# Kernel optimization log

Hardware: AMD Instinct MI355X
Metric: run time of the kernel (lower is better)

Reference implementation:

```python
import jax, jax.numpy as jnp
import numpy as np

N = 16384; E = 262144; B = 32; H = 128; R = 50; L = 4; CUTOFF = 5.0

def _lin(x, w, b):
    return x @ w + b

def _mlp2(x, w1, b1, w2, b2):
    return _lin(jax.nn.silu(_lin(x, w1, b1)), w2, b2)

def _ln(x, g, b):
    m = x.mean(-1, keepdims=True)
    v = ((x - m) ** 2).mean(-1, keepdims=True)
    return (x - m) / jnp.sqrt(v + 1e-5) * g + b

def setup_inputs() -> dict:
    key = jax.random.key(0)
    ks = iter(jax.random.split(key, 64))
    def w(shape):
        fan = shape[-2] if len(shape) >= 2 else shape[-1]
        return jax.random.normal(next(ks), shape, jnp.float32) / np.sqrt(fan)
    z = lambda shape: jnp.zeros(shape, jnp.float32)
    return {
        'atomic_numbers': jax.random.randint(next(ks), (N,), 0, 100, dtype=jnp.int32),
        'pos': 2.0 * jax.random.normal(next(ks), (N, 3), jnp.float32),
        'batch': jnp.sort(jax.random.randint(next(ks), (N,), 0, B, dtype=jnp.int32)),
        'edge_index': jax.random.randint(next(ks), (2, E), 0, N, dtype=jnp.int32),
        'embed': w((100, H)),
        'widths': jnp.full((R,), 0.5, jnp.float32),
        'ee_w1': w((L, R, H)), 'ee_b1': z((L, H)), 'ee_w2': w((L, H, H)), 'ee_b2': z((L, H)),
        'msg_w1': w((L, 3 * H, H)), 'msg_b1': z((L, H)), 'msg_w2': w((L, H, H)), 'msg_b2': z((L, H)),
        'gate_w': w((L, H, H)), 'gate_b': z((L, H)),
        'upd_w1': w((L, 2 * H, H)), 'upd_b1': z((L, H)), 'upd_w2': w((L, H, H)), 'upd_b2': z((L, H)),
        'ln_g': jnp.ones((L, H), jnp.float32), 'ln_b': z((L, H)),
        'gp_w1': w((H, H)), 'gp_b1': z((H,)), 'gp_w2': w((H, 1)), 'gp_b2': z((1,)),
        'pn_w': w((H, H)), 'pn_b': z((H,)),
        'ro_w1': w((H, H)), 'ro_b1': z((H,)), 'ro_w2': w((H, H)), 'ro_b2': z((H,)),
    }

def reference(atomic_numbers, pos, batch, edge_index, embed, widths,
              ee_w1, ee_b1, ee_w2, ee_b2, msg_w1, msg_b1, msg_w2, msg_b2,
              gate_w, gate_b, upd_w1, upd_b1, upd_w2, upd_b2, ln_g, ln_b,
              gp_w1, gp_b1, gp_w2, gp_b2, pn_w, pn_b, ro_w1, ro_b1, ro_w2, ro_b2):
    src, dst = edge_index[0], edge_index[1]  # x_j = x[src], x_i = x[dst]
    x = embed[atomic_numbers]                          # [N,H]
    # GaussianBasis RBF with cosine cutoff
    d = jnp.linalg.norm(pos[dst] - pos[src], axis=-1)[:, None]  # [E,1]
    centers = jnp.linspace(0.0, CUTOFF, R)
    gamma = 1.0 / (2.0 * widths ** 2)
    rbf = jnp.exp(-gamma * (d - centers) ** 2)
    cut = 0.5 * (jnp.cos(np.pi * d / CUTOFF) + 1.0) * (d < CUTOFF).astype(x.dtype)
    edge_attr = rbf * cut                              # [E,R]
    feats = [x]
    for l in range(L):
        ee = _mlp2(edge_attr, ee_w1[l], ee_b1[l], ee_w2[l], ee_b2[l])          # [E,H]
        m_in = jnp.concatenate([x[dst], x[src], ee], axis=-1)                   # [E,3H]
        msg = _mlp2(m_in, msg_w1[l], msg_b1[l], msg_w2[l], msg_b2[l])           # [E,H]
        gate = jax.nn.sigmoid(_lin(ee, gate_w[l], gate_b[l]))
        aggr = jax.ops.segment_sum(msg * gate, dst, num_segments=N)             # [N,H]
        upd = _mlp2(jnp.concatenate([aggr, x], axis=-1), upd_w1[l], upd_b1[l], upd_w2[l], upd_b2[l])
        x = _ln(x + upd, ln_g[l], ln_b[l])
        feats.append(x)
    atom_features = (feats[-3] + feats[-2] + feats[-1]) / 3.0                   # mean of last 3
    atom_embeddings = _mlp2(atom_features, ro_w1, ro_b1, ro_w2, ro_b2)
    # AttentionalAggregation: softmax(gate_nn(x)) over nodes per graph, weighted sum of nn(x)
    g = _lin(jnp.tanh(_lin(atom_embeddings, gp_w1, gp_b1)), gp_w2, gp_b2)[:, 0] # [N]
    gmax = jax.ops.segment_max(g, batch, num_segments=B)
    gmax = jnp.where(jnp.isfinite(gmax), gmax, 0.0)
    ex = jnp.exp(g - gmax[batch])
    den = jax.ops.segment_sum(ex, batch, num_segments=B)
    alpha = ex / den[batch]
    h = jax.nn.silu(_lin(atom_embeddings, pn_w, pn_b))
    graph_atom_features = jax.ops.segment_sum(alpha[:, None] * h, batch, num_segments=B)
    return atom_features, atom_embeddings, graph_atom_features
```

## Files before the change

### kernel.cpp

```cpp
#include <hip/hip_runtime.h>

#define NN   16384
#define NE   262144
#define NB   32
#define H    128
#define NH   (NN*H)
#define RBF  50
#define TM   64
#define KC   64
#define KP   72
#define HBP  136
#define CHW  9216
#define LT2  115712
#define LN_  49152
#define NG   196608
#define EPB  128
#define WEV  32
#define TT   4096
#define PB   32

typedef unsigned short u16;
typedef short bf16x8 __attribute__((ext_vector_type(8)));
typedef float f32x4 __attribute__((ext_vector_type(4)));
typedef float f32x16 __attribute__((ext_vector_type(16)));
// ... 40 lines not shown
  x = q.x; y = q.y;
#else
  int l_ = (int)(threadIdx.x & 63);
  unsigned as_ = __shfl(a, l_^32);
  unsigned bs_ = __shfl(b, l_^32);
  x = (l_ < 32) ? a : bs_;
  y = (l_ < 32) ? as_ : b;
#endif
}

__device__ __forceinline__ void pack_frags(const float* v, uint4& f0, uint4& f1){
  unsigned P0 = pk2(v[0],v[1]),   P1 = pk2(v[2],v[3]);
  unsigned P2 = pk2(v[4],v[5]),   P3 = pk2(v[6],v[7]);
  unsigned P4 = pk2(v[8],v[9]),   P5 = pk2(v[10],v[11]);
  unsigned P6 = pk2(v[12],v[13]), P7 = pk2(v[14],v[15]);
  unsigned x0,y0,x1,y1,x2,y2,x3,y3;
  plswap(P0,P2,x0,y0); plswap(P1,P3,x1,y1);
  plswap(P4,P6,x2,y2); plswap(P5,P7,x3,y3);
  f0.x=x0; f0.y=x1; f0.z=y0; f0.w=y1;
  f1.x=x2; f1.y=x3; f1.z=y2; f1.w=y3;
}

__device__ __forceinline__ void gll16(const u16* g, u16* l){
  __builtin_amdgcn_global_load_lds((const __attribute__((address_space(1))) void*)g,
                                   (__attribute__((address_space(3))) void*)l, 16, 0, 0);
}
__device__ __forceinline__ void gll4(const u16* g, u16* l){
  __builtin_amdgcn_global_load_lds((const __attribute__((address_space(1))) void*)g,
                                   (__attribute__((address_space(3))) void*)l, 4, 0, 0);
}

__global__ void k_zero(float* __restrict__ p, int n){
  int i = blockIdx.x*256 + threadIdx.x; if (i < n) p[i] = 0.f;
}
__global__ void k_zero_i(int* __restrict__ p, int n){
  int i = blockIdx.x*256 + threadIdx.x; if (i < n) p[i] = 0;
}
__global__ void k_embed(const int* __restrict__ z, const float* __restrict__ emb,
                        float* __restrict__ x, u16* __restrict__ xb){
  int i = blockIdx.x*256 + threadIdx.x;
  int n = i >> 7, h = i & 127;
  float v = emb[z[n]*H + h];
  x[i] = v; xb[i] = f2bf(v);
}

__global__ void k_pack(const float* __restrict__ ee_w1, const float* __restrict__ ee_w2,
                       const float* __restrict__ msg_w1, const float* __restrict__ msg_w2,
                       const float* __restrict__ gate_w, u16* __restrict__ out){
  int idx = blockIdx.x*256 + threadIdx.x;
  int l = blockIdx.y;
  if (idx >= LT2) return;
  u16* o = out + (size_t)l*LT2;
  float v = 0.f;
  if (idx < 82944){
    int c = idx / CHW, r = idx % CHW, row = r / 72, col = r % 72;
    if (col < 64){
      if (c == 0)      v = (col < RBF) ? ee_w1[(size_t)l*RBF*H + col*H + row] : 0.f;
      else if (c <= 2) v = ee_w2 [(size_t)l*H*H + (64*(c-1)+col)*H + row];
      else if (c <= 4) v = msg_w1[(size_t)l*3*H*H + (256 + 64*(c-3)+col)*H + row];
      else if (c <= 6) v = gate_w[(size_t)l*H*H + (64*(c-5)+col)*H + row];
      else             v = msg_w2[(size_t)l*H*H + (64*(c-7)+col)*H + row];
    }
  } else if (idx < 99328){
    int j = idx - 82944; int row = j >> 7, k = j & 127;
    v = msg_w1[(size_t)l*3*H*H + k*H + row];
  } else {
    int j = idx - 99328; int row = j >> 7, k = j & 127;
    v = msg_w1[(size_t)l*3*H*H + (128+k)*H + row];
  }
  o[idx] = f2bf(v);
}

__global__ void k_packn(const float* __restrict__ upd_w1, const float* __restrict__ upd_w2,
                        const float* __restrict__ ro_w1, const float* __restrict__ ro_w2,
                        const float* __restrict__ pn_w, const float* __restrict__ gp_w1,
                        u16* __restrict__ out){
  int idx = blockIdx.x*256 + threadIdx.x;
  if (idx >= NG + 65536) return;
  float v;
  if (idx < NG){
    int l = idx / LN_, j = idx % LN_;
    if (j < 32768){ int c = j>>8, k = j&255; v = upd_w1[(size_t)l*256*H + k*H + c]; }
    else { int j2 = j-32768; int c = j2>>7, k = j2&127; v = upd_w2[(size_t)l*H*H + k*H + c]; }
  } else {
    int j = idx - NG; int m = j >> 14; int j2 = j & 16383;
    int c = j2>>7, k = j2&127;
    const float* W = (m==0) ? ro_w1 : (m==1) ? ro_w2 : (m==2) ? pn_w : gp_w1;
    v = W[k*H + c];
  }
  out[idx] = f2bf(v);
}

__global__ void k_hist(const int* __restrict__ dstv, int* __restrict__ cnt){
  int e = blockIdx.x*256 + threadIdx.x;
  if (e < NE) atomicAdd(&cnt[dstv[e]], 1);
}
__global__ __launch_bounds__(1024)
void k_scan(int* __restrict__ cnt, int* __restrict__ start){
  __shared__ int ps[1024];
  int tid = threadIdx.x;
  int base = tid*16;
  int loc[16]; int s = 0;
#pragma unroll
  for (int i=0;i<16;i++){ loc[i] = s; s += cnt[base+i]; }
  ps[tid] = s; __syncthreads();
  for (int off=1; off<1024; off<<=1){
    int v = (tid>=off) ? ps[tid-off] : 0;
    __syncthreads();
    ps[tid] += v;
    __syncthreads();
  }
  int pre = (tid>0) ? ps[tid-1] : 0;
#pragma unroll
  for (int i=0;i<16;i++){ int v = pre + loc[i]; start[base+i] = v; cnt[base+i] = v; }
  if (tid == 0) start[NN] = NE;
}
__global__ void k_scatter(const int* __restrict__ srcv, const int* __restrict__ dstv,
                          int* __restrict__ cursor, int* __restrict__ src_s,
                          int* __restrict__ dst_s){
  int e = blockIdx.x*256 + threadIdx.x;
  if (e >= NE) return;
  int d = dstv[e];
  int p = atomicAdd(&cursor[d], 1);
  src_s[p] = srcv[e]; dst_s[p] = d;
}

#define TMFMA(CHP, AOFF, ACC) \
  _Pragma("unroll") \
  for (int ks_=0; ks_<64; ks_+=32){ \
    bf16x8 bf_ = *(const bf16x8*)&Ab[wrow + l15][(AOFF) + ks_ + q8]; \
    _Pragma("unroll") \
    for (int t_=0;t_<8;t_++){ \
      bf16x8 wf_ = *(const bf16x8*)&(CHP)[(t_*16 + l15)*72 + ks_ + q8]; \
      ACC[t_] = __builtin_amdgcn_mfma_f32_16x16x32_bf16(wf_, bf_, ACC[t_], 0, 0, 0); \
    } \
  }

__global__ __launch_bounds__(256)
void k_table(const u16* __restrict__ packw, const float* __restrict__ widths,
             const float* __restrict__ ee_b1, const float* __restrict__ ee_b2,
             const float* __restrict__ gate_b,
// ... 37 lines not shown
    uint4 u1; u1.x=vv[4]; u1.y=vv[5]; u1.z=vv[6]; u1.w=vv[7];
    *(uint4*)&Ab[r][k0]   = u0;
    *(uint4*)&Ab[r][k0+8] = u1;
  }
  __syncthreads();
  f32x4 acc[8];
#pragma unroll
  for (int t=0;t<8;t++) acc[t] = (f32x4)(0.f);
  TMFMA(CH[0], 0, acc)
  const int s = rowbase + wrow + l15;
#pragma unroll
  for (int t=0;t<8;t++){
    int co = t*16 + quad*4;
    int po = (co>>6)*KP + (co&63);
    *(uint2*)&Ab[wrow + l15][po] = pack4(
      siluf_(acc[t][0]+b1s[co]),   siluf_(acc[t][1]+b1s[co+1]),
      siluf_(acc[t][2]+b1s[co+2]), siluf_(acc[t][3]+b1s[co+3]));
  }
#pragma unroll
  for (int t=0;t<8;t++) acc[t] = (f32x4)(0.f);
  TMFMA(CH[1], 0, acc)
  TMFMA(CH[2], KP, acc)
#pragma unroll
  for (int t=0;t<8;t++){
    int co = t*16 + quad*4;
    int po = (co>>6)*KP + (co&63);
    *(uint2*)&Ab[wrow + l15][po] = pack4(
      acc[t][0]+b2s[co], acc[t][1]+b2s[co+1], acc[t][2]+b2s[co+2], acc[t][3]+b2s[co+3]);
  }
#pragma unroll
  for (int t=0;t<8;t++) acc[t] = (f32x4)(0.f);
  TMFMA(CH[3], 0, acc)
  TMFMA(CH[4], KP, acc)
#pragma unroll
  for (int t=0;t<8;t++){
    int co = t*16 + quad*4;
    *(uint2*)&m1t[((size_t)lyr*TT + s)*H + permc(co)] =
      pack4(acc[t][0], acc[t][1], acc[t][2], acc[t][3]);
  }
#pragma unroll
  for (int t=0;t<8;t++) acc[t] = (f32x4)(0.f);
  TMFMA(CH[5], 0, acc)
  TMFMA(CH[6], KP, acc)
#pragma unroll
  for (int t=0;t<8;t++){
    int co = t*16 + quad*4;
    *(uint2*)&gt[((size_t)lyr*TT + s)*H + permc(co)] = pack4(
      sigmoidf_(acc[t][0]+bgs[co]),   sigmoidf_(acc[t][1]+bgs[co+1]),
      sigmoidf_(acc[t][2]+bgs[co+2]), sigmoidf_(acc[t][3]+bgs[co+3]));
  }
}


#define GSTAGE(cidx, dbuf) { \
  const u16* gs_ = pw + (size_t)(cidx)*CHW; \
  u16* ls_ = &UN[(dbuf)*CHW]; \
  _Pragma("unroll") \
  for (int i_=0;i_<4;i_++) \
    gll16(gs_ + (i_*256 + tid)*8, ls_ + (i_*256 + tid)*8); \
  _Pragma("unroll") \
  for (int i_=0;i_<2;i_++) \
    gll4(gs_ + 8192 + (i_*256 + tid)*2, ls_ + 8192 + (i_*256 + tid)*2); \
}

#define ECHUNK32(WB, FR, ACC) \
  _Pragma("unroll") \
  for (int s_=0; s_<4; s_++){ \
    bf16x8 bf_ = __builtin_bit_cast(bf16x8, (FR)[s_]); \
    _Pragma("unroll") \
    for (int t_=0;t_<4;t_++){ \
      bf16x8 wf_ = *(const bf16x8*)&(WB)[(t_*32 + l31)*72 + s_*16 + hi8]; \
      ACC[t_] = __builtin_amdgcn_mfma_f32_32x32x16_bf16(wf_, bf_, ACC[t_], 0, 0, 0); \
    } \
  }

#define ZACC(A) { _Pragma("unroll") for (int z_=0;z_<4;z_++) A[z_] = (f32x16)(0.f); }

#define SEL2(V, UF) (((UF)&1) ? make_uint2((V).z,(V).w) : make_uint2((V).x,(V).y))

#define DWEL(r) (((r)&3)==0 ? dw[(r)>>2].x : ((r)&3)==1 ? dw[(r)>>2].y : \
                 ((r)&3)==2 ? dw[(r)>>2].z : dw[(r)>>2].w)

__global__ __launch_bounds__(256, 3)
void k_edge(const int* __restrict__ src_s, const int* __restrict__ dst_s,
            const float* __restrict__ pos,
            const u16* __restrict__ y1b, const u16* __restrict__ y2b,
            const u16* __restrict__ pw,
            const u16* __restrict__ m1t, const u16* __restrict__ gt,
            const float* __restrict__ b_m2, float* __restrict__ aggr){
  __shared__ __align__(16) u16 UN[2*CHW];
  __shared__ float BM[H];
  const int tid = threadIdx.x;
  const int wave = tid>>6, l = tid&63, l31 = l&31, hi = l>>5, hi8 = hi*8;
  const int ebase = blockIdx.x*EPB + wave*WEV;
  const int eid   = ebase + l31;
  if (tid < H) BM[tid] = b_m2[tid];

  const int esrc = src_s[eid], edst = dst_s[eid];
  float dx = pos[3*edst]   - pos[3*esrc];
  float dy = pos[3*edst+1] - pos[3*esrc+1];
  float dz = pos[3*edst+2] - pos[3*esrc+2];
  float dist = sqrtf(dx*dx + dy*dy + dz*dz);
  float uu = fminf(dist, 5.0f) * ((float)(TT-1)/5.0f);
  int i0 = (int)uu; if (i0 > TT-2) i0 = TT-2;
  float w = uu - (float)i0;

  const u16* yp1 = y1b + (size_t)edst*H + hi*64;
  const u16* yp2 = y2b + (size_t)esrc*H + hi*64;
  const u16* mp  = m1t + (size_t)i0*H  + hi*64;
  uint4 Y1[8], Y2[8], M0[8], M1[8];
#pragma unroll
  for (int i=0;i<8;i++){
    Y1[i] = *(const uint4*)&yp1[i*8];
    Y2[i] = *(const uint4*)&yp2[i*8];
    M0[i] = *(const uint4*)&mp[i*8];
    M1[i] = *(const uint4*)&mp[H + i*8];
  }

  GSTAGE(0,0)
  GSTAGE(1,1)

  uint4 fmh[8];
#pragma unroll
  for (int tf=0;tf<4;tf++){
    float v_[16];
#pragma unroll
    for (int uf=0;uf<4;uf++){
      int iv = 2*tf + (uf>>1);
      uint2 a1 = SEL2(Y1[iv],uf), a2 = SEL2(Y2[iv],uf);
      uint2 m0 = SEL2(M0[iv],uf), m1 = SEL2(M1[iv],uf);
      float p0 = blo(m0.x), p1 = bhi(m0.x), p2 = blo(m0.y), p3 = bhi(m0.y);
      float q0 = blo(m1.x), q1 = bhi(m1.x), q2 = blo(m1.y), q3 = bhi(m1.y);
      v_[4*uf+0] = siluf_(fmaf(w, q0-p0, p0) + blo(a1.x) + blo(a2.x));
      v_[4*uf+1] = siluf_(fmaf(w, q1-p1, p1) + bhi(a1.x) + bhi(a2.x));
      v_[4*uf+2] = siluf_(fmaf(w, q2-p2, p2) + blo(a1.y) + blo(a2.y));
      v_[4*uf+3] = siluf_(fmaf(w, q3-p3, p3) + bhi(a1.y) + bhi(a2.y));
    }
    pack_frags(v_, fmh[2*tf], fmh[2*tf+1]);
  }

  __syncthreads();

  const u16* gp = gt + (size_t)i0*H + hi*64;
  uint4 G0[8], G1[8];
#pragma unroll
  for (int i=0;i<8;i++){
    G0[i] = *(const uint4*)&gp[i*8];
    G1[i] = *(const uint4*)&gp[H + i*8];
  }

  f32x16 acc[4];
  ZACC(acc)
  ECHUNK32((&UN[0]),   fmh,   acc)
  ECHUNK32((&UN[CHW]), fmh+4, acc)

  __syncthreads();
  u16* Sb = &UN[wave*(WEV*HBP)];

#pragma unroll
  for (int tf=0;tf<4;tf++){
#pragma unroll
    for (int uf=0;uf<4;uf++){
      int iv = 2*tf + (uf>>1);
      int co = 32*tf + 4*hi + 8*uf;
      float4 bm = *(const float4*)&BM[co];
      uint2 a0 = SEL2(G0[iv],uf), a1 = SEL2(G1[iv],uf);
      float g0 = fmaf(w, blo(a1.x)-blo(a0.x), blo(a0.x));
      float g1 = fmaf(w, bhi(a1.x)-bhi(a0.x), bhi(a0.x));
      float g2 = fmaf(w, blo(a1.y)-blo(a0.y), blo(a0.y));
      float g3 = fmaf(w, bhi(a1.y)-bhi(a0.y), bhi(a0.y));
      float m0 = (acc[tf][4*uf+0]+bm.x)*g0;
      float m1 = (acc[tf][4*uf+1]+bm.y)*g1;
      float m2 = (acc[tf][4*uf+2]+bm.z)*g2;
      float m3 = (acc[tf][4*uf+3]+bm.w)*g3;
      *(uint2*)&Sb[l31*HBP + co] = pack4(m0, m1, m2, m3);
    }
  }

  {
    int4 dw[8];
#pragma unroll
    for (int i=0;i<8;i++) dw[i] = *(const int4*)&dst_s[ebase + 4*i];
    int c0 = l*2;
    float a0 = 0.f, a1 = 0.f;
    int cur = dw[0].x;
#pragma unroll
    for (int r=0;r<32;r++){
      int d = DWEL(r);
      if (d != cur){
        atomicAdd(&aggr[(size_t)cur*H + c0],     a0);
        atomicAdd(&aggr[(size_t)cur*H + c0 + 1], a1);
        a0 = 0.f; a1 = 0.f; cur = d;
      }
      unsigned pv = *(const unsigned*)&Sb[r*HBP + c0];
      a0 += blo(pv); a1 += bhi(pv);
    }
    atomicAdd(&aggr[(size_t)cur*H + c0],     a0);
    atomicAdd(&aggr[(size_t)cur*H + c0 + 1], a1);
  }
}


#define NMFMA(AB, WB, NP, ACC) \
  _Pragma("unroll") \
  for (int kk_=0; kk_<(NP)*64; kk_+=32){ \
    int po_ = (kk_>>6)*KP + (kk_&63); \
    bf16x8 bf_ = *(const bf16x8*)&AB[wrow + l15][po_ + q8]; \
    _Pragma("unroll") \
    for (int t_=0;t_<8;t_++){ \
      bf16x8 wf_ = *(const bf16x8*)&WB[t_*16 + l15][po_ + q8]; \
      ACC[t_] = __builtin_amdgcn_mfma_f32_16x16x32_bf16(wf_, bf_, ACC[t_], 0, 0, 0); \
    } \
  }

#define NMFMA2(AB, AOFF, WB_, WOFF, ACC) \
  _Pragma("unroll") \
  for (int kk_=0; kk_<64; kk_+=32){ \
    bf16x8 bf_ = *(const bf16x8*)&AB[wrow + l15][(AOFF) + kk_ + q8]; \
    _Pragma("unroll") \
    for (int t_=0;t_<8;t_++){ \
      bf16x8 wf_ = *(const bf16x8*)&WB_[t_*16 + l15][(WOFF) + kk_ + q8]; \
      ACC[t_] = __builtin_amdgcn_mfma_f32_16x16x32_bf16(wf_, bf_, ACC[t_], 0, 0, 0); \
    } \
  }

#define NSTAGE_W2(WB_, GSRC, KPAD, SP, DP) \
  _Pragma("unroll") \
  for (int i_=0;i_<4;i_++){ \
    int o_ = tid + i_*256; int c_ = o_>>3, ko_ = (o_&7)*8; \
    *(uint4*)&WB_[c_][(DP)*KP + ko_] = *(const uint4*)((GSRC) + (size_t)c_*(KPAD) + (SP)*64 + ko_); \
  }
#define NSTAGE_W(WB, GSRC, KPAD, P) NSTAGE_W2(WB, GSRC, KPAD, P, P)

#define NSTAGE_A(AB, GSRC, P) \
  _Pragma("unroll") \
  for (int i_=0;i_<2;i_++){ \
    int o_ = tid*2 + i_; int r_ = o_>>3, ko_ = (o_&7)*8; \
    *(uint4*)&AB[r_][(P)*KP + ko_] = *(const uint4*)((GSRC) + (size_t)r_*H + (P)*64 + ko_); \
  }

#define NSTAGE_AF(AB, GSRC, P) \
  _Pragma("unroll") \
  for (int i_=0;i_<2;i_++){ \
    int o_ = tid*2 + i_; int r_ = o_>>3, ko_ = (o_&7)*8; \
    const float* rp_ = (GSRC) + (size_t)r_*H + (P)*64 + ko_; \
    float4 f0_ = *(const float4*)rp_; \
    float4 f1_ = *(const float4*)(rp_ + 4); \
    uint4 pk_; \
    pk_.x = pk2(f0_.x, f0_.y); pk_.y = pk2(f0_.z, f0_.w); \
    pk_.z = pk2(f1_.x, f1_.y); pk_.w = pk2(f1_.z, f1_.w); \
    *(uint4*)&AB[r_][(P)*KP + ko_] = pk_; \
  }

__global__ __launch_bounds__(256)
void k_y12(const u16* __restrict__ xb, const u16* __restrict__ Wd,
           const u16* __restrict__ Ws, const float* __restrict__ b1,
           u16* __restrict__ y1, u16* __restrict__ y2){
  __shared__ u16 Ab[TM][2*KP];
  __shared__ u16 W1[H][2*KP];
  __shared__ u16 W2[H][2*KP];
  __shared__ float bls[H];
  const int tid = threadIdx.x;
  const int wave = tid>>6, l = tid&63, l15 = l&15, quad = l>>4;
  const int wrow = wave*16, q8 = quad*8;
  const int rowbase = blockIdx.x*TM;
  if (tid < H) bls[tid] = b1[tid];
  NSTAGE_W(W1, Wd, 128, 0) NSTAGE_W(W1, Wd, 128, 1)
  NSTAGE_W(W2, Ws, 128, 0) NSTAGE_W(W2, Ws, 128, 1)
  NSTAGE_A(Ab, xb + (size_t)rowbase*H, 0) NSTAGE_A(Ab, xb + (size_t)rowbase*H, 1)
  __syncthreads();
  f32x4 a1[8], a2[8];
#pragma unroll
  for (int t=0;t<8;t++){ a1[t] = (f32x4)(0.f); a2[t] = (f32x4)(0.f); }
  NMFMA(Ab, W1, 2, a1)
  NMFMA(Ab, W2, 2, a2)
  const int node = rowbase + wrow + l15;
#pragma unroll
  for (int t=0;t<8;t++){
    int co = t*16 + quad*4;
    int pc = permc(co);
    *(uint2*)&y1[(size_t)node*H + pc] = pack4(
      a1[t][0]+bls[co], a1[t][1]+bls[co+1], a1[t][2]+bls[co+2], a1[t][3]+bls[co+3]);
    *(uint2*)&y2[(size_t)node*H + pc] = pack4(
      a2[t][0], a2[t][1], a2[t][2], a2[t][3]);
  }
}

template<int ADDSUM, int DOY12>
__global__ __launch_bounds__(256)
void k_upd(float* __restrict__ aggr, const u16* __restrict__ xin,
           const u16* __restrict__ W1p, const float* __restrict__ b1,
           const u16* __restrict__ W2p, const float* __restrict__ b2,
           const float* __restrict__ lng, const float* __restrict__ lnb,
           float* __restrict__ x, float* __restrict__ sumf, u16* __restrict__ xb,
           const u16* __restrict__ Wdn, const u16* __restrict__ Wsn,
           const float* __restrict__ b1n,
           u16* __restrict__ y1, u16* __restrict__ y2){
  __shared__ u16 Ab[TM][4*KP];
  __shared__ u16 WB[3][H][2*KP];
  __shared__ float bls[H], b2s[H], lgs[H], lbs[H], b1s[H];
  const int tid = threadIdx.x;
  const int wave = tid>>6, l = tid&63, l15 = l&15, quad = l>>4;
  const int wrow = wave*16, q8 = quad*8;
  const int rowbase = blockIdx.x*TM;
  if (tid < H){ bls[tid] = b1[tid]; b2s[tid] = b2[tid]; lgs[tid] = lng[tid];
                if (DOY12) b1s[tid] = b1n[tid]; }
  else lbs[tid-H] = lnb[tid-H];
  NSTAGE_W2(WB[0], W1p, 256, 0, 0) NSTAGE_W2(WB[0], W1p, 256, 1, 1)
  NSTAGE_W2(WB[1], W1p, 256, 2, 0) NSTAGE_W2(WB[1], W1p, 256, 3, 1)
  NSTAGE_W2(WB[2], W2p, 128, 0, 0) NSTAGE_W2(WB[2], W2p, 128, 1, 1)
  NSTAGE_AF(Ab, aggr + (size_t)rowbase*H, 0)
  NSTAGE_AF(Ab, aggr + (size_t)rowbase*H, 1)
  {
    const u16* xs = xin + (size_t)rowbase*H - 128;
    NSTAGE_A(Ab, xs, 2) NSTAGE_A(Ab, xs, 3)
  }
  __syncthreads();
  f32x4 acc[8];
#pragma unroll
  for (int t=0;t<8;t++) acc[t] = (f32x4)(0.f);
  NMFMA2(Ab, 0,    WB[0], 0,  acc)
  NMFMA2(Ab, KP,   WB[0], KP, acc)
  NMFMA2(Ab, 2*KP, WB[1], 0,  acc)
  NMFMA2(Ab, 3*KP, WB[1], KP, acc)
  {
    float4 z = make_float4(0.f,0.f,0.f,0.f);
#pragma unroll
    for (int i=0;i<8;i++){
      int o = tid + i*256;
      *(float4*)&aggr[(size_t)rowbase*H + (size_t)o*4] = z;
    }
  }
#pragma unroll
  for (int t=0;t<8;t++){
    int co = t*16 + quad*4;
    int po = (co>>6)*KP + (co&63);
    *(uint2*)&Ab[wrow + l15][po] = pack4(
      siluf_(acc[t][0]+bls[co]),   siluf_(acc[t][1]+bls[co+1]),
      siluf_(acc[t][2]+bls[co+2]), siluf_(acc[t][3]+bls[co+3]));
  }
  __syncthreads();
  if (DOY12){
    NSTAGE_W2(WB[0], Wdn, 128, 0, 0) NSTAGE_W2(WB[0], Wdn, 128, 1, 1)
    NSTAGE_W2(WB[1], Wsn, 128, 0, 0) NSTAGE_W2(WB[1], Wsn, 128, 1, 1)
  }
#pragma unroll
  for (int t=0;t<8;t++) acc[t] = (f32x4)(0.f);
  NMFMA2(Ab, 0,  WB[2], 0,  acc)
  NMFMA2(Ab, KP, WB[2], KP, acc)
  const int node = rowbase + wrow + l15;
  const size_t ro = (size_t)node*H;
  float y[8][4]; float s = 0.f, ss = 0.f;
#pragma unroll
  for (int t=0;t<8;t++){
    int co = t*16 + quad*4;
    float4 xv = *(const float4*)&x[ro + co];
    y[t][0] = xv.x + acc[t][0] + b2s[co];
    y[t][1] = xv.y + acc[t][1] + b2s[co+1];
    y[t][2] = xv.z + acc[t][2] + b2s[co+2];
    y[t][3] = xv.w + acc[t][3] + b2s[co+3];
#pragma unroll
    for (int r=0;r<4;r++){ s += y[t][r]; ss += y[t][r]*y[t][r]; }
  }
  s  += __shfl_xor(s, 16);  s  += __shfl_xor(s, 32);
  ss += __shfl_xor(ss, 16); ss += __shfl_xor(ss, 32);
  float mean = s*(1.0f/H);
  float var  = ss*(1.0f/H) - mean*mean;
  float inv  = rsqrtf(var + 1e-5f);
#pragma unroll
  for (int t=0;t<8;t++){
    int co = t*16 + quad*4;
    float4 o;
    o.x = (y[t][0]-mean)*inv*lgs[co]   + lbs[co];
    o.y = (y[t][1]-mean)*inv*lgs[co+1] + lbs[co+1];
    o.z = (y[t][2]-mean)*inv*lgs[co+2] + lbs[co+2];
    o.w = (y[t][3]-mean)*inv*lgs[co+3] + lbs[co+3];
    *(float4*)&x[ro + co] = o;
    if (ADDSUM){
      float4 sf = *(const float4*)&sumf[ro + co];
      sf.x += o.x*(1.0f/3.0f); sf.y += o.y*(1.0f/3.0f);
      sf.z += o.z*(1.0f/3.0f); sf.w += o.w*(1.0f/3.0f);
      *(float4*)&sumf[ro + co] = sf;
      if (!DOY12)
        *(uint2*)&y1[ro + co] = pack4(sf.x, sf.y, sf.z, sf.w);
    }
    *(uint2*)&xb[ro + co] = pack4(o.x, o.y, o.z, o.w);
    y[t][0] = o.x; y[t][1] = o.y; y[t][2] = o.z; y[t][3] = o.w;
  }

  if (DOY12){
#pragma unroll
    for (int t=0;t<8;t++){
      int co = t*16 + quad*4;
      int po = (2 + (co>>6))*KP + (co&63);
      *(uint2*)&Ab[wrow + l15][po] = pack4(y[t][0], y[t][1], y[t][2], y[t][3]);
    }
    __syncthreads();
    f32x4 a1[8], a2[8];
#pragma unroll
    for (int t=0;t<8;t++){ a1[t] = (f32x4)(0.f); a2[t] = (f32x4)(0.f); }
    NMFMA2(Ab, 2*KP, WB[0], 0,  a1)
    NMFMA2(Ab, 3*KP, WB[0], KP, a1)
    NMFMA2(Ab, 2*KP, WB[1], 0,  a2)
    NMFMA2(Ab, 3*KP, WB[1], KP, a2)
#pragma unroll
    for (int t=0;t<8;t++){
      int co = t*16 + quad*4;
      int pc = permc(co);
      *(uint2*)&y1[ro + pc] = pack4(
        a1[t][0]+b1s[co], a1[t][1]+b1s[co+1], a1[t][2]+b1s[co+2], a1[t][3]+b1s[co+3]);
      *(uint2*)&y2[ro + pc] = pack4(a2[t][0], a2[t][1], a2[t][2], a2[t][3]);
    }
  }
}

__global__ __launch_bounds__(256)
void k_tail(const u16* __restrict__ afb,
            const u16* __restrict__ Wro1, const float* __restrict__ bro1,
            const u16* __restrict__ Wro2, const float* __restrict__ bro2,
            const u16* __restrict__ Wpn,  const float* __restrict__ bpn,
            const u16* __restrict__ Wgp,  const float* __restrict__ bgp,
            const float* __restrict__ w2, const float* __restrict__ b2g,
            float* __restrict__ out_ae, u16* __restrict__ hb,
            float* __restrict__ g){
  __shared__ u16 Ab[TM][2*KP];
  __shared__ u16 WB[3][H][2*KP];
  __shared__ float r1b[H], r2b[H], pnb[H], g1b[H], w2s[H];
  const int tid = threadIdx.x;
  const int wave = tid>>6, l = tid&63, l15 = l&15, quad = l>>4;
  const int wrow = wave*16, q8 = quad*8;
  const int rowbase = blockIdx.x*TM;
  if (tid < H){ r1b[tid]=bro1[tid]; r2b[tid]=bro2[tid]; pnb[tid]=bpn[tid]; g1b[tid]=bgp[tid]; }
  else w2s[tid-H] = w2[tid-H];
  NSTAGE_W(WB[0], Wro1, 128, 0) NSTAGE_W(WB[0], Wro1, 128, 1)
  NSTAGE_W(WB[1], Wro2, 128, 0) NSTAGE_W(WB[1], Wro2, 128, 1)
  NSTAGE_W(WB[2], Wpn,  128, 0) NSTAGE_W(WB[2], Wpn,  128, 1)
  NSTAGE_A(Ab, afb + (size_t)rowbase*H, 0) NSTAGE_A(Ab, afb + (size_t)rowbase*H, 1)
  __syncthreads();
  f32x4 acc[8];
#pragma unroll
  for (int t=0;t<8;t++) acc[t] = (f32x4)(0.f);
  NMFMA2(Ab, 0, WB[0], 0, acc) NMFMA2(Ab, KP, WB[0], KP, acc)
#pragma unroll
  for (int t=0;t<8;t++){
    int co = t*16 + quad*4;
    int po = (co>>6)*KP + (co&63);
    *(uint2*)&Ab[wrow + l15][po] = pack4(
      siluf_(acc[t][0]+r1b[co]),   siluf_(acc[t][1]+r1b[co+1]),
      siluf_(acc[t][2]+r1b[co+2]), siluf_(acc[t][3]+r1b[co+3]));
  }
  __syncthreads();
  NSTAGE_W(WB[0], Wgp, 128, 0) NSTAGE_W(WB[0], Wgp, 128, 1)
#pragma unroll
  for (int t=0;t<8;t++) acc[t] = (f32x4)(0.f);
  NMFMA2(Ab, 0, WB[1], 0, acc) NMFMA2(Ab, KP, WB[1], KP, acc)
  const int node = rowbase + wrow + l15;
  const size_t ro = (size_t)node*H;
#pragma unroll
  for (int t=0;t<8;t++){
    int co = t*16 + quad*4;
    float v0 = acc[t][0]+r2b[co],   v1 = acc[t][1]+r2b[co+1];
    float v2 = acc[t][2]+r2b[co+2], v3 = acc[t][3]+r2b[co+3];
    float4 o; o.x=v0; o.y=v1; o.z=v2; o.w=v3;
    *(float4*)&out_ae[ro + co] = o;
    int po = (co>>6)*KP + (co&63);
    *(uint2*)&Ab[wrow + l15][po] = pack4(v0,v1,v2,v3);
  }
  asm volatile("s_waitcnt lgkmcnt(0)" ::: "memory");
#pragma unroll
  for (int t=0;t<8;t++) acc[t] = (f32x4)(0.f);
  NMFMA2(Ab, 0, WB[2], 0, acc) NMFMA2(Ab, KP, WB[2], KP, acc)
#pragma unroll
  for (int t=0;t<8;t++){
    int co = t*16 + quad*4;
    *(uint2*)&hb[ro + co] = pack4(
      siluf_(acc[t][0]+pnb[co]),   siluf_(acc[t][1]+pnb[co+1]),
      siluf_(acc[t][2]+pnb[co+2]), siluf_(acc[t][3]+pnb[co+3]));
  }
  __syncthreads();
#pragma unroll
  for (int t=0;t<8;t++) acc[t] = (f32x4)(0.f);
  NMFMA2(Ab, 0, WB[0], 0, acc) NMFMA2(Ab, KP, WB[0], KP, acc)
  float p = 0.f;
#pragma unroll
  for (int t=0;t<8;t++){
    int co = t*16 + quad*4;
#pragma unroll
    for (int r=0;r<4;r++) p = fmaf(tanhf(acc[t][r]+g1b[co+r]), w2s[co+r], p);
  }
  p += __shfl_xor(p, 16); p += __shfl_xor(p, 32);
  if (quad == 0) g[node] = p + b2g[0];
}

__global__ void k_start(const int* __restrict__ batch, int* __restrict__ start){
  int b = threadIdx.x;
  if (b > NB) return;
  if (b == NB){ start[NB] = NN; return; }
  int lo = 0, hi = NN;
  while (lo < hi){ int mid = (lo+hi) >> 1; if (batch[mid] < b) lo = mid+1; else hi = mid; }
  start[b] = lo;
}

__global__ __launch_bounds__(256)
void k_pool(const int* __restrict__ start, const float* __restrict__ g,
            const u16* __restrict__ hb, float* __restrict__ out){
  const int b   = blockIdx.x / PB;
  const int sub = blockIdx.x % PB;
  const int s = start[b], e = start[b+1];
  const int tid = threadIdx.x;
  __shared__ float red[4];
  __shared__ float s_gmax, s_den;
  __shared__ float part[2][H];

  float mx = -1e30f;
  for (int n = s + tid; n < e; n += 256) mx = fmaxf(mx, g[n]);
#pragma unroll
  for (int m=32;m>=1;m>>=1) mx = fmaxf(mx, __shfl_xor(mx, m, 64));
  if ((tid & 63) == 0) red[tid >> 6] = mx;
  __syncthreads();
  if (tid == 0){
    float v = fmaxf(fmaxf(red[0],red[1]), fmaxf(red[2],red[3]));
    s_gmax = (e > s) ? v : 0.0f;
  }
  __syncthreads();
  const float gmax = s_gmax;

  float sum = 0.f;
  for (int n = s + tid; n < e; n += 256) sum += __expf(g[n] - gmax);
#pragma unroll
  for (int m=32;m>=1;m>>=1) sum += __shfl_xor(sum, m, 64);
  if ((tid & 63) == 0) red[tid >> 6] = sum;
  __syncthreads();
  if (tid == 0) s_den = red[0]+red[1]+red[2]+red[3];
  __syncthreads();
  const float den = s_den;
// ... 48 lines not shown
  const float* gp_b2  = (const float*)d_in[25];
  const float* pn_w   = (const float*)d_in[26];
  const float* pn_b   = (const float*)d_in[27];
  const float* ro_w1  = (const float*)d_in[28];
  const float* ro_b1  = (const float*)d_in[29];
  const float* ro_w2  = (const float*)d_in[30];
  const float* ro_b2  = (const float*)d_in[31];

  const int* srcv = ei;
  const int* dstv = ei + NE;

  char* p0 = (char*)d_ws;
  char* p = p0;
  auto carve = [&](size_t bytes)->char*{ char* q = p; p += (bytes + 63) & ~(size_t)63; return q; };
  float* x     = (float*)carve((size_t)NH*4);
  float* aggr  = (float*)carve((size_t)NH*4);
  float* gsc   = (float*)carve((size_t)NN*4);
  float* exb   = (float*)carve((size_t)NN*4);
  int*   startb  = (int*)carve((size_t)(NB+2)*4);
  int*   estart  = (int*)carve((size_t)(NN+1)*4);
  int*   ecursor = (int*)carve((size_t)NN*4);
  int*   src_s   = (int*)carve((size_t)NE*4);
  int*   dst_s   = (int*)carve((size_t)NE*4);
  u16*   xb      = (u16*)carve((size_t)NH*2);
  u16*   packw   = (u16*)carve((size_t)4*LT2*2);
  u16*   packn   = (u16*)carve((size_t)(NG+65536)*2);
  u16*   nb1     = (u16*)carve((size_t)NH*2);
  u16*   nb2     = (u16*)carve((size_t)NH*2);
  u16*   m1tab   = (u16*)carve((size_t)4*TT*H*2);
  u16*   gtab    = (u16*)carve((size_t)4*TT*H*2);

  float* out_af  = (float*)d_out;
  float* out_ae  = out_af + NH;
  float* out_gaf = out_ae + NH;

  k_pack<<<dim3((LT2+255)/256, 4), 256, 0, stream>>>(ee_w1, ee_w2, msg_w1, msg_w2, gate_w, packw);
  k_packn<<<(NG+65536+255)/256, 256, 0, stream>>>(upd_w1, upd_w2, ro_w1, ro_w2, pn_w, gp_w1, packn);
  k_table<<<dim3(TT/TM, 4), 256, 0, stream>>>(packw, widths, ee_b1, ee_b2, gate_b, m1tab, gtab);
  k_zero_i<<<(NN+255)/256, 256, 0, stream>>>(ecursor, NN);
  k_hist<<<NE/256, 256, 0, stream>>>(dstv, ecursor);
  k_scan<<<1, 1024, 0, stream>>>(ecursor, estart);
  k_scatter<<<NE/256, 256, 0, stream>>>(srcv, dstv, ecursor, src_s, dst_s);
  k_embed<<<NH/256, 256, 0, stream>>>(Z, embed, x, xb);
  k_zero<<<NH/256, 256, 0, stream>>>(out_af, NH);
  k_zero<<<(NB*H+255)/256, 256, 0, stream>>>(out_gaf, NB*H);
  k_zero<<<NH/256, 256, 0, stream>>>(aggr, NH);

  k_y12<<<NN/TM, 256, 0, stream>>>(xb, packw + 82944, packw + 99328, msg_b1, nb1, nb2);

  for (int l=0; l<4; l++){
    const u16* pwn = packn + (size_t)l*LN_;
    const u16* pwN = packw + (size_t)(l+1)*LT2;
    k_edge<<<NE/EPB, 256, 0, stream>>>(src_s, dst_s, pos, nb1, nb2,
                                       packw + (size_t)l*LT2 + (size_t)7*CHW,
                                       m1tab + (size_t)l*TT*H, gtab + (size_t)l*TT*H,
                                       msg_b2 + l*H, aggr);
    if (l == 0)
      k_upd<0,1><<<NN/TM, 256, 0, stream>>>(aggr, xb, pwn, upd_b1 + l*H,
                                            pwn + 32768, upd_b2 + l*H,
                                            ln_g + l*H, ln_b + l*H, x, out_af, xb,
                                            pwN + 82944, pwN + 99328, msg_b1 + (l+1)*H,
                                            nb1, nb2);
    else if (l < 3)
      k_upd<1,1><<<NN/TM, 256, 0, stream>>>(aggr, xb, pwn, upd_b1 + l*H,
                                            pwn + 32768, upd_b2 + l*H,
                                            ln_g + l*H, ln_b + l*H, x, out_af, xb,
                                            pwN + 82944, pwN + 99328, msg_b1 + (l+1)*H,
                                            nb1, nb2);
    else
      k_upd<1,0><<<NN/TM, 256, 0, stream>>>(aggr, xb, pwn, upd_b1 + l*H,
                                            pwn + 32768, upd_b2 + l*H,
                                            ln_g + l*H, ln_b + l*H, x, out_af, xb,
                                            packw, packw, msg_b1,
                                            nb1, nb2);
  }

  k_tail<<<NN/TM, 256, 0, stream>>>(nb1,
                                    packn + NG,         ro_b1,
                                    packn + NG + 16384, ro_b2,
                                    packn + NG + 32768, pn_b,
                                    packn + NG + 49152, gp_b1, gp_w2, gp_b2,
                                    out_ae, nb2, gsc);
  k_start<<<1, 64, 0, stream>>>(batch, startb);
  k_pool<<<NB*PB, 256, 0, stream>>>(startb, gsc, nb2, out_gaf);
}
```

Baseline: 536.7 us.

## Pre-pack weights in MFMA fragment order and read them directly from global

The pack kernels now emit weight matrices already arranged in per-lane MFMA fragment order. The edge, y12, update and tail kernels read weight fragments straight from global memory (L1/L2 cached) instead of staging them into shared memory. This removes the LDS staging copies and several block barriers, and shrinks shared memory so more blocks can be resident (launch bounds raised to 2 blocks per CU). The cost is repeated per-wave global or cache reads of the same weights in every block, which adds L2 traffic, especially in the edge kernel.

```diff
diff --git a/kernel.cpp b/kernel.cpp
--- a/kernel.cpp
+++ b/kernel.cpp
@@ -116,21 +116,34 @@
   if (idx >= LT2) return;
   u16* o = out + (size_t)l*LT2;
   float v = 0.f;
-  if (idx < 82944){
+  if (idx < 64512){
     int c = idx / CHW, r = idx % CHW, row = r / 72, col = r % 72;
     if (col < 64){
       if (c == 0)      v = (col < RBF) ? ee_w1[(size_t)l*RBF*H + col*H + row] : 0.f;
       else if (c <= 2) v = ee_w2 [(size_t)l*H*H + (64*(c-1)+col)*H + row];
       else if (c <= 4) v = msg_w1[(size_t)l*3*H*H + (256 + 64*(c-3)+col)*H + row];
-      else if (c <= 6) v = gate_w[(size_t)l*H*H + (64*(c-5)+col)*H + row];
-      else             v = msg_w2[(size_t)l*H*H + (64*(c-7)+col)*H + row];
-    }
+      else             v = gate_w[(size_t)l*H*H + (64*(c-5)+col)*H + row];
+    }
+  } else if (idx < 64512 + 16384){
+    int r = idx - 64512; int c = r >> 13; int rr = r & 8191;
+    int jj = rr&7, ll = (rr>>3)&63, tt = (rr>>9)&3, ss = (rr>>11)&3;
+    int col = tt*32 + (ll&31);
+    int k = c*64 + ss*16 + (ll>>5)*8 + jj;
+    v = msg_w2[(size_t)l*H*H + k*H + col];
+  } else if (idx < 82944){
+    v = 0.f;
   } else if (idx < 99328){
-    int j = idx - 82944; int row = j >> 7, k = j & 127;
-    v = msg_w1[(size_t)l*3*H*H + k*H + row];
+    int j2 = idx - 82944;
+    int jj=j2&7, ll=(j2>>3)&63, tt=(j2>>9)&7, ks=(j2>>12)&1, pp=j2>>13;
+    int k = pp*64 + ks*32 + (ll>>4)*8 + jj;
+    int col = tt*16 + (ll&15);
+    v = msg_w1[(size_t)l*3*H*H + k*H + col];
   } else {
-    int j = idx - 99328; int row = j >> 7, k = j & 127;
-    v = msg_w1[(size_t)l*3*H*H + (128+k)*H + row];
+    int j2 = idx - 99328;
+    int jj=j2&7, ll=(j2>>3)&63, tt=(j2>>9)&7, ks=(j2>>12)&1, pp=j2>>13;
+    int k = pp*64 + ks*32 + (ll>>4)*8 + jj;
+    int col = tt*16 + (ll&15);
+    v = msg_w1[(size_t)l*3*H*H + (128+k)*H + col];
   }
   o[idx] = f2bf(v);
 }
@@ -144,13 +157,25 @@
   float v;
   if (idx < NG){
     int l = idx / LN_, j = idx % LN_;
-    if (j < 32768){ int c = j>>8, k = j&255; v = upd_w1[(size_t)l*256*H + k*H + c]; }
-    else { int j2 = j-32768; int c = j2>>7, k = j2&127; v = upd_w2[(size_t)l*H*H + k*H + c]; }
+    if (j < 32768){
+      int jj=j&7, ll=(j>>3)&63, tt=(j>>9)&7, ks=(j>>12)&1, pp=j>>13;
+      int k = pp*64 + ks*32 + (ll>>4)*8 + jj;
+      int col = tt*16 + (ll&15);
+      v = upd_w1[(size_t)l*256*H + k*H + col];
+    } else {
+      int j2 = j - 32768;
+      int jj=j2&7, ll=(j2>>3)&63, tt=(j2>>9)&7, ks=(j2>>12)&1, pp=j2>>13;
+      int k = pp*64 + ks*32 + (ll>>4)*8 + jj;
+      int col = tt*16 + (ll&15);
+      v = upd_w2[(size_t)l*H*H + k*H + col];
+    }
   } else {
     int j = idx - NG; int m = j >> 14; int j2 = j & 16383;
-    int c = j2>>7, k = j2&127;
+    int jj=j2&7, ll=(j2>>3)&63, tt=(j2>>9)&7, ks=(j2>>12)&1, pp=j2>>13;
+    int k = pp*64 + ks*32 + (ll>>4)*8 + jj;
+    int col = tt*16 + (ll&15);
     const float* W = (m==0) ? ro_w1 : (m==1) ? ro_w2 : (m==2) ? pn_w : gp_w1;
-    v = W[k*H + c];
+    v = W[k*H + col];
   }
   out[idx] = f2bf(v);
 }
@@ -294,32 +319,8 @@
 }
 
 
-#define GSTAGE(cidx, dbuf) { \
-  const u16* gs_ = pw + (size_t)(cidx)*CHW; \
-  u16* ls_ = &UN[(dbuf)*CHW]; \
-  _Pragma("unroll") \
-  for (int i_=0;i_<4;i_++) \
-    gll16(gs_ + (i_*256 + tid)*8, ls_ + (i_*256 + tid)*8); \
-  _Pragma("unroll") \
-  for (int i_=0;i_<2;i_++) \
-    gll4(gs_ + 8192 + (i_*256 + tid)*2, ls_ + 8192 + (i_*256 + tid)*2); \
-}
-
-#define ECHUNK32(WB, FR, ACC) \
-  _Pragma("unroll") \
-  for (int s_=0; s_<4; s_++){ \
-    bf16x8 bf_ = __builtin_bit_cast(bf16x8, (FR)[s_]); \
-    _Pragma("unroll") \
-    for (int t_=0;t_<4;t_++){ \
-      bf16x8 wf_ = *(const bf16x8*)&(WB)[(t_*32 + l31)*72 + s_*16 + hi8]; \
-      ACC[t_] = __builtin_amdgcn_mfma_f32_32x32x16_bf16(wf_, bf_, ACC[t_], 0, 0, 0); \
-    } \
-  }
-
 #define ZACC(A) { _Pragma("unroll") for (int z_=0;z_<4;z_++) A[z_] = (f32x16)(0.f); }
-
 #define SEL2(V, UF) (((UF)&1) ? make_uint2((V).z,(V).w) : make_uint2((V).x,(V).y))
-
 #define DWEL(r) (((r)&3)==0 ? dw[(r)>>2].x : ((r)&3)==1 ? dw[(r)>>2].y : \
                  ((r)&3)==2 ? dw[(r)>>2].z : dw[(r)>>2].w)
 
@@ -330,12 +331,13 @@
             const u16* __restrict__ pw,
             const u16* __restrict__ m1t, const u16* __restrict__ gt,
             const float* __restrict__ b_m2, float* __restrict__ aggr){
-  __shared__ __align__(16) u16 UN[2*CHW];
+  __shared__ u16 SB[4][WEV][HBP];
   __shared__ float BM[H];
   const int tid = threadIdx.x;
-  const int wave = tid>>6, l = tid&63, l31 = l&31, hi = l>>5, hi8 = hi*8;
+  const int wave = tid>>6, l = tid&63, l31 = l&31, hi = l>>5;
   const int ebase = blockIdx.x*EPB + wave*WEV;
   const int eid   = ebase + l31;
+  u16 (*Sb)[HBP] = SB[wave];
   if (tid < H) BM[tid] = b_m2[tid];
 
   const int esrc = src_s[eid], edst = dst_s[eid];
@@ -359,8 +361,7 @@
     M1[i] = *(const uint4*)&mp[H + i*8];
   }
 
-  GSTAGE(0,0)
-  GSTAGE(1,1)
+  __syncthreads();
 
   uint4 fmh[8];
 #pragma unroll
@@ -381,8 +382,6 @@
     pack_frags(v_, fmh[2*tf], fmh[2*tf+1]);
   }
 
-  __syncthreads();
-
   const u16* gp = gt + (size_t)i0*H + hi*64;
   uint4 G0[8], G1[8];
 #pragma unroll
@@ -393,11 +392,18 @@
 
   f32x16 acc[4];
   ZACC(acc)
-  ECHUNK32((&UN[0]),   fmh,   acc)
-  ECHUNK32((&UN[CHW]), fmh+4, acc)
-
-  __syncthreads();
-  u16* Sb = &UN[wave*(WEV*HBP)];
+#pragma unroll
+  for (int c=0;c<2;c++){
+#pragma unroll
+    for (int s_=0;s_<4;s_++){
+      bf16x8 bf_ = __builtin_bit_cast(bf16x8, fmh[c*4+s_]);
+#pragma unroll
+      for (int t_=0;t_<4;t_++){
+        bf16x8 wf_ = *(const bf16x8*)&pw[((c*16 + s_*4 + t_)*64 + l)*8];
+        acc[t_] = __builtin_amdgcn_mfma_f32_32x32x16_bf16(wf_, bf_, acc[t_], 0, 0, 0);
+      }
+    }
+  }
 
 #pragma unroll
   for (int tf=0;tf<4;tf++){
@@ -415,7 +421,7 @@
       float m1 = (acc[tf][4*uf+1]+bm.y)*g1;
       float m2 = (acc[tf][4*uf+2]+bm.z)*g2;
       float m3 = (acc[tf][4*uf+3]+bm.w)*g3;
-      *(uint2*)&Sb[l31*HBP + co] = pack4(m0, m1, m2, m3);
+      *(uint2*)&Sb[l31][co] = pack4(m0, m1, m2, m3);
     }
   }
 
@@ -434,7 +440,7 @@
         atomicAdd(&aggr[(size_t)cur*H + c0 + 1], a1);
         a0 = 0.f; a1 = 0.f; cur = d;
       }
-      unsigned pv = *(const unsigned*)&Sb[r*HBP + c0];
+      unsigned pv = *(const unsigned*)&Sb[r][c0];
       a0 += blo(pv); a1 += bhi(pv);
     }
     atomicAdd(&aggr[(size_t)cur*H + c0],     a0);
@@ -443,36 +449,19 @@
 }
 
 
-#define NMFMA(AB, WB, NP, ACC) \
+#define GFMFMA(GW, APB, NP, ACC) \
   _Pragma("unroll") \
-  for (int kk_=0; kk_<(NP)*64; kk_+=32){ \
-    int po_ = (kk_>>6)*KP + (kk_&63); \
-    bf16x8 bf_ = *(const bf16x8*)&AB[wrow + l15][po_ + q8]; \
+  for (int p_=0;p_<(NP);p_++){ \
     _Pragma("unroll") \
-    for (int t_=0;t_<8;t_++){ \
-      bf16x8 wf_ = *(const bf16x8*)&WB[t_*16 + l15][po_ + q8]; \
-      ACC[t_] = __builtin_amdgcn_mfma_f32_16x16x32_bf16(wf_, bf_, ACC[t_], 0, 0, 0); \
+    for (int ks_=0;ks_<2;ks_++){ \
+      bf16x8 bf_ = *(const bf16x8*)&Ab[wrow + l15][((APB)+p_)*KP + ks_*32 + q8]; \
+      _Pragma("unroll") \
+      for (int t_=0;t_<8;t_++){ \
+        bf16x8 wf_ = *(const bf16x8*)&(GW)[((((p_*2+ks_)*8)+t_)*64 + l)*8]; \
+        ACC[t_] = __builtin_amdgcn_mfma_f32_16x16x32_bf16(wf_, bf_, ACC[t_], 0, 0, 0); \
+      } \
     } \
   }
-
-#define NMFMA2(AB, AOFF, WB_, WOFF, ACC) \
-  _Pragma("unroll") \
-  for (int kk_=0; kk_<64; kk_+=32){ \
-    bf16x8 bf_ = *(const bf16x8*)&AB[wrow + l15][(AOFF) + kk_ + q8]; \
-    _Pragma("unroll") \
-    for (int t_=0;t_<8;t_++){ \
-      bf16x8 wf_ = *(const bf16x8*)&WB_[t_*16 + l15][(WOFF) + kk_ + q8]; \
-      ACC[t_] = __builtin_amdgcn_mfma_f32_16x16x32_bf16(wf_, bf_, ACC[t_], 0, 0, 0); \
-    } \
-  }
-
-#define NSTAGE_W2(WB_, GSRC, KPAD, SP, DP) \
-  _Pragma("unroll") \
-  for (int i_=0;i_<4;i_++){ \
-    int o_ = tid + i_*256; int c_ = o_>>3, ko_ = (o_&7)*8; \
-    *(uint4*)&WB_[c_][(DP)*KP + ko_] = *(const uint4*)((GSRC) + (size_t)c_*(KPAD) + (SP)*64 + ko_); \
-  }
-#define NSTAGE_W(WB, GSRC, KPAD, P) NSTAGE_W2(WB, GSRC, KPAD, P, P)
 
 #define NSTAGE_A(AB, GSRC, P) \
   _Pragma("unroll") \
@@ -494,28 +483,24 @@
     *(uint4*)&AB[r_][(P)*KP + ko_] = pk_; \
   }
 
-__global__ __launch_bounds__(256)
+__global__ __launch_bounds__(256, 2)
 void k_y12(const u16* __restrict__ xb, const u16* __restrict__ Wd,
            const u16* __restrict__ Ws, const float* __restrict__ b1,
            u16* __restrict__ y1, u16* __restrict__ y2){
   __shared__ u16 Ab[TM][2*KP];
-  __shared__ u16 W1[H][2*KP];
-  __shared__ u16 W2[H][2*KP];
   __shared__ float bls[H];
   const int tid = threadIdx.x;
   const int wave = tid>>6, l = tid&63, l15 = l&15, quad = l>>4;
   const int wrow = wave*16, q8 = quad*8;
   const int rowbase = blockIdx.x*TM;
   if (tid < H) bls[tid] = b1[tid];
-  NSTAGE_W(W1, Wd, 128, 0) NSTAGE_W(W1, Wd, 128, 1)
-  NSTAGE_W(W2, Ws, 128, 0) NSTAGE_W(W2, Ws, 128, 1)
   NSTAGE_A(Ab, xb + (size_t)rowbase*H, 0) NSTAGE_A(Ab, xb + (size_t)rowbase*H, 1)
   __syncthreads();
   f32x4 a1[8], a2[8];
 #pragma unroll
   for (int t=0;t<8;t++){ a1[t] = (f32x4)(0.f); a2[t] = (f32x4)(0.f); }
-  NMFMA(Ab, W1, 2, a1)
-  NMFMA(Ab, W2, 2, a2)
+  GFMFMA(Wd, 0, 2, a1)
+  GFMFMA(Ws, 0, 2, a2)
   const int node = rowbase + wrow + l15;
 #pragma unroll
   for (int t=0;t<8;t++){
@@ -529,17 +514,16 @@
 }
 
 template<int ADDSUM, int DOY12>
-__global__ __launch_bounds__(256)
+__global__ __launch_bounds__(256, 2)
 void k_upd(float* __restrict__ aggr, const u16* __restrict__ xin,
-           const u16* __restrict__ W1p, const float* __restrict__ b1,
-           const u16* __restrict__ W2p, const float* __restrict__ b2,
+           const u16* __restrict__ W1g, const float* __restrict__ b1,
+           const u16* __restrict__ W2g, const float* __restrict__ b2,
            const float* __restrict__ lng, const float* __restrict__ lnb,
            float* __restrict__ x, float* __restrict__ sumf, u16* __restrict__ xb,
            const u16* __restrict__ Wdn, const u16* __restrict__ Wsn,
            const float* __restrict__ b1n,
            u16* __restrict__ y1, u16* __restrict__ y2){
   __shared__ u16 Ab[TM][4*KP];
-  __shared__ u16 WB[3][H][2*KP];
   __shared__ float bls[H], b2s[H], lgs[H], lbs[H], b1s[H];
   const int tid = threadIdx.x;
   const int wave = tid>>6, l = tid&63, l15 = l&15, quad = l>>4;
@@ -548,9 +532,6 @@
   if (tid < H){ bls[tid] = b1[tid]; b2s[tid] = b2[tid]; lgs[tid] = lng[tid];
                 if (DOY12) b1s[tid] = b1n[tid]; }
   else lbs[tid-H] = lnb[tid-H];
-  NSTAGE_W2(WB[0], W1p, 256, 0, 0) NSTAGE_W2(WB[0], W1p, 256, 1, 1)
-  NSTAGE_W2(WB[1], W1p, 256, 2, 0) NSTAGE_W2(WB[1], W1p, 256, 3, 1)
-  NSTAGE_W2(WB[2], W2p, 128, 0, 0) NSTAGE_W2(WB[2], W2p, 128, 1, 1)
   NSTAGE_AF(Ab, aggr + (size_t)rowbase*H, 0)
   NSTAGE_AF(Ab, aggr + (size_t)rowbase*H, 1)
   {
@@ -561,10 +542,7 @@
   f32x4 acc[8];
 #pragma unroll
   for (int t=0;t<8;t++) acc[t] = (f32x4)(0.f);
-  NMFMA2(Ab, 0,    WB[0], 0,  acc)
-  NMFMA2(Ab, KP,   WB[0], KP, acc)
-  NMFMA2(Ab, 2*KP, WB[1], 0,  acc)
-  NMFMA2(Ab, 3*KP, WB[1], KP, acc)
+  GFMFMA(W1g, 0, 4, acc)
   {
     float4 z = make_float4(0.f,0.f,0.f,0.f);
 #pragma unroll
@@ -581,15 +559,9 @@
       siluf_(acc[t][0]+bls[co]),   siluf_(acc[t][1]+bls[co+1]),
       siluf_(acc[t][2]+bls[co+2]), siluf_(acc[t][3]+bls[co+3]));
   }
-  __syncthreads();
-  if (DOY12){
-    NSTAGE_W2(WB[0], Wdn, 128, 0, 0) NSTAGE_W2(WB[0], Wdn, 128, 1, 1)
-    NSTAGE_W2(WB[1], Wsn, 128, 0, 0) NSTAGE_W2(WB[1], Wsn, 128, 1, 1)
-  }
-#pragma unroll
-  for (int t=0;t<8;t++) acc[t] = (f32x4)(0.f);
-  NMFMA2(Ab, 0,  WB[2], 0,  acc)
-  NMFMA2(Ab, KP, WB[2], KP, acc)
+#pragma unroll
+  for (int t=0;t<8;t++) acc[t] = (f32x4)(0.f);
+  GFMFMA(W2g, 0, 2, acc)
   const int node = rowbase + wrow + l15;
   const size_t ro = (size_t)node*H;
   float y[8][4]; float s = 0.f, ss = 0.f;
@@ -637,14 +609,11 @@
       int po = (2 + (co>>6))*KP + (co&63);
       *(uint2*)&Ab[wrow + l15][po] = pack4(y[t][0], y[t][1], y[t][2], y[t][3]);
     }
-    __syncthreads();
     f32x4 a1[8], a2[8];
 #pragma unroll
     for (int t=0;t<8;t++){ a1[t] = (f32x4)(0.f); a2[t] = (f32x4)(0.f); }
-    NMFMA2(Ab, 2*KP, WB[0], 0,  a1)
-    NMFMA2(Ab, 3*KP, WB[0], KP, a1)
-    NMFMA2(Ab, 2*KP, WB[1], 0,  a2)
-    NMFMA2(Ab, 3*KP, WB[1], KP, a2)
+    GFMFMA(Wdn, 2, 2, a1)
+    GFMFMA(Wsn, 2, 2, a2)
 #pragma unroll
     for (int t=0;t<8;t++){
       int co = t*16 + quad*4;
@@ -656,7 +625,7 @@
   }
 }
 
-__global__ __launch_bounds__(256)
+__global__ __launch_bounds__(256, 2)
 void k_tail(const u16* __restrict__ afb,
             const u16* __restrict__ Wro1, const float* __restrict__ bro1,
             const u16* __restrict__ Wro2, const float* __restrict__ bro2,
@@ -666,7 +635,6 @@
             float* __restrict__ out_ae, u16* __restrict__ hb,
             float* __restrict__ g){
   __shared__ u16 Ab[TM][2*KP];
-  __shared__ u16 WB[3][H][2*KP];
   __shared__ float r1b[H], r2b[H], pnb[H], g1b[H], w2s[H];
   const int tid = threadIdx.x;
   const int wave = tid>>6, l = tid&63, l15 = l&15, quad = l>>4;
@@ -674,15 +642,12 @@
   const int rowbase = blockIdx.x*TM;
   if (tid < H){ r1b[tid]=bro1[tid]; r2b[tid]=bro2[tid]; pnb[tid]=bpn[tid]; g1b[tid]=bgp[tid]; }
   else w2s[tid-H] = w2[tid-H];
-  NSTAGE_W(WB[0], Wro1, 128, 0) NSTAGE_W(WB[0], Wro1, 128, 1)
-  NSTAGE_W(WB[1], Wro2, 128, 0) NSTAGE_W(WB[1], Wro2, 128, 1)
-  NSTAGE_W(WB[2], Wpn,  128, 0) NSTAGE_W(WB[2], Wpn,  128, 1)
   NSTAGE_A(Ab, afb + (size_t)rowbase*H, 0) NSTAGE_A(Ab, afb + (size_t)rowbase*H, 1)
   __syncthreads();
   f32x4 acc[8];
 #pragma unroll
   for (int t=0;t<8;t++) acc[t] = (f32x4)(0.f);
-  NMFMA2(Ab, 0, WB[0], 0, acc) NMFMA2(Ab, KP, WB[0], KP, acc)
+  GFMFMA(Wro1, 0, 2, acc)
 #pragma unroll
   for (int t=0;t<8;t++){
     int co = t*16 + quad*4;
@@ -691,11 +656,9 @@
       siluf_(acc[t][0]+r1b[co]),   siluf_(acc[t][1]+r1b[co+1]),
       siluf_(acc[t][2]+r1b[co+2]), siluf_(acc[t][3]+r1b[co+3]));
   }
-  __syncthreads();
-  NSTAGE_W(WB[0], Wgp, 128, 0) NSTAGE_W(WB[0], Wgp, 128, 1)
-#pragma unroll
-  for (int t=0;t<8;t++) acc[t] = (f32x4)(0.f);
-  NMFMA2(Ab, 0, WB[1], 0, acc) NMFMA2(Ab, KP, WB[1], KP, acc)
+#pragma unroll
+  for (int t=0;t<8;t++) acc[t] = (f32x4)(0.f);
+  GFMFMA(Wro2, 0, 2, acc)
   const int node = rowbase + wrow + l15;
   const size_t ro = (size_t)node*H;
 #pragma unroll
@@ -708,10 +671,9 @@
     int po = (co>>6)*KP + (co&63);
     *(uint2*)&Ab[wrow + l15][po] = pack4(v0,v1,v2,v3);
   }
-  asm volatile("s_waitcnt lgkmcnt(0)" ::: "memory");
-#pragma unroll
-  for (int t=0;t<8;t++) acc[t] = (f32x4)(0.f);
-  NMFMA2(Ab, 0, WB[2], 0, acc) NMFMA2(Ab, KP, WB[2], KP, acc)
+#pragma unroll
+  for (int t=0;t<8;t++) acc[t] = (f32x4)(0.f);
+  GFMFMA(Wpn, 0, 2, acc)
 #pragma unroll
   for (int t=0;t<8;t++){
     int co = t*16 + quad*4;
@@ -719,10 +681,9 @@
       siluf_(acc[t][0]+pnb[co]),   siluf_(acc[t][1]+pnb[co+1]),
       siluf_(acc[t][2]+pnb[co+2]), siluf_(acc[t][3]+pnb[co+3]));
   }
-  __syncthreads();
-#pragma unroll
-  for (int t=0;t<8;t++) acc[t] = (f32x4)(0.f);
-  NMFMA2(Ab, 0, WB[0], 0, acc) NMFMA2(Ab, KP, WB[0], KP, acc)
+#pragma unroll
+  for (int t=0;t<8;t++) acc[t] = (f32x4)(0.f);
+  GFMFMA(Wgp, 0, 2, acc)
   float p = 0.f;
 #pragma unroll
   for (int t=0;t<8;t++){
@@ -877,7 +838,7 @@
     const u16* pwn = packn + (size_t)l*LN_;
     const u16* pwN = packw + (size_t)(l+1)*LT2;
     k_edge<<<NE/EPB, 256, 0, stream>>>(src_s, dst_s, pos, nb1, nb2,
-                                       packw + (size_t)l*LT2 + (size_t)7*CHW,
+                                       packw + (size_t)l*LT2 + 64512,
                                        m1tab + (size_t)l*TT*H, gtab + (size_t)l*TT*H,
                                        msg_b2 + l*H, aggr);
     if (l == 0)
```

Result: slower. 641.0 us (+19.4%).
